# Kernel optimization log

Measured on AMD Instinct MI355X. Metric: run time of the kernel, lower is better.

The kernel has to match this reference:

```python
import jax, jax.numpy as jnp
import numpy as np

N = 50000
E = 640000
IN_DIM = 23
HID = 128
NUM_CLASS = 12


def setup_inputs() -> dict:
    key = jax.random.key(0)
    ks = jax.random.split(key, 12)
    x = jax.random.normal(ks[0], (N, IN_DIM), dtype=jnp.float32)
    edge_index = jax.random.randint(ks[1], (2, E), 0, N, dtype=jnp.int32)

    def glorot(k, shape):
        fan_in, fan_out = shape
        lim = np.sqrt(6.0 / (fan_in + fan_out)).astype(np.float32)
        return jax.random.uniform(k, shape, jnp.float32, -lim, lim)

    W1 = glorot(ks[2], (IN_DIM, HID)); b1 = jnp.zeros((HID,), jnp.float32)
    W2 = glorot(ks[3], (HID, HID));    b2 = jnp.zeros((HID,), jnp.float32)
    W3 = glorot(ks[4], (HID, HID));    b3 = jnp.zeros((HID,), jnp.float32)
    Wc1 = glorot(ks[5], (HID, 64));    bc1 = jnp.zeros((64,), jnp.float32)
    Wc2 = glorot(ks[6], (64, NUM_CLASS)); bc2 = jnp.zeros((NUM_CLASS,), jnp.float32)
    return {"x": x, "edge_index": edge_index,
            "W1": W1, "b1": b1, "W2": W2, "b2": b2, "W3": W3, "b3": b3,
            "Wc1": Wc1, "bc1": bc1, "Wc2": Wc2, "bc2": bc2}


def _gcn_norm(edge_index, n_nodes):
    # add self loops, compute symmetric normalization D^-1/2 (A+I) D^-1/2
    loop = jnp.arange(n_nodes, dtype=edge_index.dtype)
    src = jnp.concatenate([edge_index[0], loop])
    dst = jnp.concatenate([edge_index[1], loop])
    deg = jax.ops.segment_sum(jnp.ones_like(dst, dtype=jnp.float32), dst,
                              num_segments=n_nodes)
    dinv = jax.lax.rsqrt(deg)  # deg >= 1 due to self loops
    norm = dinv[src] * dinv[dst]  # [E + N]
    return src, dst, norm


def _gcn_layer(h, W, b, src, dst, norm, n_nodes):
    h = h @ W                          # linear (bias applied after aggregation, per PyG)
    msg = h[src] * norm[:, None]       # gather + scale
    out = jax.ops.segment_sum(msg, dst, num_segments=n_nodes)  # scatter-add
    return out + b


def reference(x, edge_index, W1, b1, W2, b2, W3, b3, Wc1, bc1, Wc2, bc2):
    n = x.shape[0]
    src, dst, norm = _gcn_norm(edge_index, n)
    h = jnp.tanh(_gcn_layer(x, W1, b1, src, dst, norm, n))
    h = jnp.tanh(_gcn_layer(h, W2, b2, src, dst, norm, n))
    h = jnp.tanh(_gcn_layer(h, W3, b3, src, dst, norm, n))
    # dropout is identity in eval mode
    out = h @ Wc1 + bc1
    out = out @ Wc2 + bc2
    return out
```

## Files before the change

### kernel.cpp

```cpp
#include <hip/hip_runtime.h>
#include <math.h>

#define NN 50000
#define EE 640000
#define IND 23
#define HID 128
#define MIDD 64
#define NCLS 12
#define NB 49
#define QS 32766.0f
#define INVQS (1.0f / 32766.0f)

typedef short short8v __attribute__((ext_vector_type(8)));
typedef float f32x4 __attribute__((ext_vector_type(4)));

__device__ __forceinline__ short f2bf(float f) {
    unsigned u = __float_as_uint(f);
    unsigned r = (u + 0x7FFFu + ((u >> 16) & 1u)) >> 16;
    return (short)r;
}
__device__ __forceinline__ float bf2f(short s) {
    return __uint_as_float(((unsigned)(unsigned short)s) << 16);
}


__global__ void k_count(const int* __restrict__ dst, int* __restrict__ cnt, int e) {
    int i = blockIdx.x * blockDim.x + threadIdx.x;
    if (i < e) atomicAdd(&cnt[dst[i]], 1);
}

__global__ __launch_bounds__(256) void k_scan_local(const int* __restrict__ cnt,
                                                    int* __restrict__ row_ptr,
                                                    float* __restrict__ dinv,
                                                    int* __restrict__ sums) {
    __shared__ int wtot[4];
    const int tid = threadIdx.x;
    const int wid = tid >> 6, lane = tid & 63;
    const int base = blockIdx.x * 1024 + tid * 4;
    int v[4];
#pragma unroll
    for (int t = 0; t < 4; ++t) {
        int i = base + t;
        v[t] = (i < NN) ? cnt[i] : 0;
        if (i < NN) dinv[i] = rsqrtf((float)v[t] + 1.0f);
    }
    int slocal = v[0] + v[1] + v[2] + v[3];
    int val = slocal;
#pragma unroll
    for (int off = 1; off < 64; off <<= 1) {
        int t = __shfl_up(val, off, 64);
        if (lane >= off) val += t;
    }
    if (lane == 63) wtot[wid] = val;
    __syncthreads();
    int woff = 0;
#pragma unroll
    for (int w = 0; w < 4; ++w) woff += (w < wid) ? wtot[w] : 0;
    int run = woff + val - slocal;
#pragma unroll
    for (int t = 0; t < 4; ++t) {
        int i = base + t;
        if (i < NN) row_ptr[i] = run;
        run += v[t];
    }
    if (tid == 255) sums[blockIdx.x] = woff + val;
}

__global__ void k_scan_sums(const int* __restrict__ sums, int* __restrict__ offs,
                            int* __restrict__ row_ptr) {
    const int lane = threadIdx.x;
    int v = (lane < NB) ? sums[lane] : 0;
    int val = v;
#pragma unroll
    for (int off = 1; off < 64; off <<= 1) {
        int t = __shfl_up(val, off, 64);
        if (lane >= off) val += t;
    }
    if (lane < NB) offs[lane] = val - v;
    if (lane == NB - 1) row_ptr[NN] = val;
}

__global__ __launch_bounds__(256) void k_scan_apply(int* __restrict__ row_ptr,
                                                    const int* __restrict__ offs,
                                                    int* __restrict__ cursor) {
    const int base = blockIdx.x * 1024 + threadIdx.x * 4;
    const int o = offs[blockIdx.x];
#pragma unroll
    for (int t = 0; t < 4; ++t) {
        int i = base + t;
        if (i < NN) {
            int rp = row_ptr[i] + o;
            row_ptr[i] = rp;
            cursor[i] = rp;
        }
    }
}

__global__ void k_fill(const int* __restrict__ src, const int* __restrict__ dst,
                       int* __restrict__ cursor, const float* __restrict__ dinv,
                       int2* __restrict__ e_sn, int e) {
    int i = blockIdx.x * blockDim.x + threadIdx.x;
    if (i < e) {
        int s = src[i];
        int d = dst[i];
        float w = dinv[s];
        int pos = atomicAdd(&cursor[d], 1);
        e_sn[pos] = make_int2(s, __float_as_int(w));
    }
}

__global__ __launch_bounds__(256) void k_pad(const float* __restrict__ x,
                                             const float* __restrict__ dinv,
                                             float* __restrict__ xp) {
    int i = blockIdx.x * 256 + threadIdx.x;
    int node = i >> 5, f = i & 31;
    xp[i] = (f < IND) ? x[node * IND + f] * dinv[node] : 0.f;
}

__global__ void k_wcc(const float* __restrict__ Wc1, const float* __restrict__ bc1,
                      const float* __restrict__ Wc2, const float* __restrict__ bc2,
                      float* __restrict__ Wcc, float* __restrict__ bcc) {
    int t = blockIdx.x * 256 + threadIdx.x;
    if (t < HID * NCLS) {
        int k = t / NCLS, c = t % NCLS;
        float s = 0.f;
#pragma unroll 8
        for (int j = 0; j < MIDD; ++j) s += Wc1[k * MIDD + j] * Wc2[j * NCLS + c];
        Wcc[t] = s;
    }
    if (t < NCLS) {
        float s = bc2[t];
#pragma unroll 8
        for (int j = 0; j < MIDD; ++j) s += bc1[j] * Wc2[j * NCLS + t];
        bcc[t] = s;
    }
}

__global__ void k_wsplit(const float* __restrict__ Wa, const float* __restrict__ Wb,
                         short* __restrict__ hiA, short* __restrict__ loA,
                         short* __restrict__ hiB, short* __restrict__ loB) {
    int i = blockIdx.x * 256 + threadIdx.x;
    const float* W = (blockIdx.y == 0) ? Wa : Wb;
    short* hi = (blockIdx.y == 0) ? hiA : hiB;
    short* lo = (blockIdx.y == 0) ? loA : loB;
    int k = i >> 7, c = i & 127;
    float w = W[i];
    short h = f2bf(w);
    short l = f2bf(w - bf2f(h));
    int t = k >> 5, g = (k >> 3) & 3, j = k & 7;
    int idx = ((t * 4 + g) * 128 + c) * 8 + j;
    hi[idx] = h;
    lo[idx] = l;
}

__global__ __launch_bounds__(256) void k_l1(const float* __restrict__ xp,
                                            const float* __restrict__ W1,
                                            const float* __restrict__ b1,
                                            const int* __restrict__ row_ptr,
                                            const int2* __restrict__ e_sn,
                                            const float* __restrict__ dinv,
                                            short* __restrict__ outq) {
    const int tid = threadIdx.x;
    const int i = blockIdx.x * 4 + (tid >> 6);
    const int lane = tid & 63;
    const int slot = lane >> 3;
    const int f = lane & 7;
    const float4* xp4 = (const float4*)xp;
    const int beg = row_ptr[i];
    const int deg = row_ptr[i + 1] - beg;
    float4 acc = make_float4(0.f, 0.f, 0.f, 0.f);
    for (int base = 0; base < deg; base += 64) {
        const int cnt = min(64, deg - base);
        int s_l = 0;
        if (lane < cnt) s_l = e_sn[beg + base + lane].x;
        int e = 0;
        for (; e + 8 <= cnt; e += 8) {
            int s = __shfl(s_l, e + slot, 64);
            float4 v = xp4[s * 8 + f];
            acc.x += v.x; acc.y += v.y; acc.z += v.z; acc.w += v.w;
        }
        if (e < cnt) {
            int s = __shfl(s_l, e + slot, 64);
            if (e + slot < cnt) {
                float4 v = xp4[s * 8 + f];
                acc.x += v.x; acc.y += v.y; acc.z += v.z; acc.w += v.w;
            }
        }
    }
#pragma unroll
    for (int off = 32; off >= 8; off >>= 1) {
        acc.x += __shfl_down(acc.x, off, 64);
        acc.y += __shfl_down(acc.y, off, 64);
        acc.z += __shfl_down(acc.z, off, 64);
        acc.w += __shfl_down(acc.w, off, 64);
    }
    const float di = dinv[i];
    if (lane < 8) {
        float4 v = xp4[i * 8 + lane];
        acc.x = (acc.x + v.x) * di; acc.y = (acc.y + v.y) * di;
        acc.z = (acc.z + v.z) * di; acc.w = (acc.w + v.w) * di;
    }
    float a0 = b1[lane], a1 = b1[lane + 64];
#pragma unroll
    for (int k = 0; k < IND; ++k) {
        float comp = ((k & 3) == 0) ? acc.x : ((k & 3) == 1) ? acc.y
                   : ((k & 3) == 2) ? acc.z : acc.w;
        float xk = __shfl(comp, k >> 2, 64);
        a0 += xk * W1[k * HID + lane];
        a1 += xk * W1[k * HID + lane + 64];
    }
    outq[i * HID + lane]      = (short)__float2int_rn(tanhf(a0) * QS);
    outq[i * HID + lane + 64] = (short)__float2int_rn(tanhf(a1) * QS);
}

__global__ __launch_bounds__(256) void k_aggq(const short* __restrict__ hq,
                                              const int* __restrict__ row_ptr,
                                              const int2* __restrict__ e_sn,
                                              const float* __restrict__ dinv,
                                              float* __restrict__ aggf) {
    const int tid = threadIdx.x;
    const int i = blockIdx.x * 4 + (tid >> 6);
    const int lane = tid & 63;
    const int slot = lane >> 4;
    const int f = lane & 15;
    const short8v* h8 = (const short8v*)hq;
    const int beg = row_ptr[i];
    const int deg = row_ptr[i + 1] - beg;
    float facc[8];
#pragma unroll
    for (int t = 0; t < 8; ++t) facc[t] = 0.f;
    for (int base = 0; base < deg; base += 64) {
        const int cnt = min(64, deg - base);
        int s_l = 0; float n_l = 0.f;
        if (lane < cnt) {
            int2 sn = e_sn[beg + base + lane];
            s_l = sn.x;
            n_l = __int_as_float(sn.y);
        }
        int e = 0;
#pragma unroll 4
        for (; e + 4 <= cnt; e += 4) {
            int s = __shfl(s_l, e + slot, 64);
            float nr = __shfl(n_l, e + slot, 64);
            short8v v = h8[s * 16 + f];
#pragma unroll
            for (int t = 0; t < 8; ++t) facc[t] += (float)v[t] * nr;
        }
        if (e < cnt) {
            int s = __shfl(s_l, e + slot, 64);
            float nr = __shfl(n_l, e + slot, 64);
            if (e + slot < cnt) {
                short8v v = h8[s * 16 + f];
#pragma unroll
                for (int t = 0; t < 8; ++t) facc[t] += (float)v[t] * nr;
            }
        }
    }
#pragma unroll
    for (int off = 32; off >= 16; off >>= 1)
#pragma unroll
        for (int t = 0; t < 8; ++t) facc[t] += __shfl_down(facc[t], off, 64);
    if (lane < 16) {
        const float di = dinv[i];
        const float sc = di * INVQS;
        short8v v = h8[i * 16 + lane];
        float4 o0, o1;
        o0.x = (facc[0] + di * (float)v[0]) * sc;
        o0.y = (facc[1] + di * (float)v[1]) * sc;
        o0.z = (facc[2] + di * (float)v[2]) * sc;
        o0.w = (facc[3] + di * (float)v[3]) * sc;
        o1.x = (facc[4] + di * (float)v[4]) * sc;
        o1.y = (facc[5] + di * (float)v[5]) * sc;
        o1.z = (facc[6] + di * (float)v[6]) * sc;
        o1.w = (facc[7] + di * (float)v[7]) * sc;
        ((float4*)aggf)[i * 32 + lane * 2]     = o0;
        ((float4*)aggf)[i * 32 + lane * 2 + 1] = o1;
    }
}

__device__ __forceinline__ void gemm_core(const float* __restrict__ hin,
                                          const short8v* __restrict__ whi8,
                                          const short8v* __restrict__ wlo8,
                                          int row, bool rv, int g, int c16,
                                          f32x4 acc[8]) {
#pragma unroll
    for (int t = 0; t < 4; ++t) {
        float4 a0 = make_float4(0.f, 0.f, 0.f, 0.f), a1 = a0;
        if (rv) {
            const float4* hp = (const float4*)&hin[row * HID + t * 32 + g * 8];
            a0 = hp[0]; a1 = hp[1];
        }
        float av[8];
        av[0] = a0.x; av[1] = a0.y; av[2] = a0.z; av[3] = a0.w;
        av[4] = a1.x; av[5] = a1.y; av[6] = a1.z; av[7] = a1.w;
        short8v ahi, alo;
#pragma unroll
        for (int j = 0; j < 8; ++j) {
            short h = f2bf(av[j]);
            ahi[j] = h;
            alo[j] = f2bf(av[j] - bf2f(h));
        }
        const int wb = (t * 4 + g) * 128 + c16;
#pragma unroll
        for (int n = 0; n < 8; ++n) {
            short8v bh = whi8[wb + n * 16];
            short8v bl = wlo8[wb + n * 16];
            acc[n] = __builtin_amdgcn_mfma_f32_16x16x32_bf16(ahi, bh, acc[n], 0, 0, 0);
            acc[n] = __builtin_amdgcn_mfma_f32_16x16x32_bf16(ahi, bl, acc[n], 0, 0, 0);
            acc[n] = __builtin_amdgcn_mfma_f32_16x16x32_bf16(alo, bh, acc[n], 0, 0, 0);
        }
    }
}

__global__ __launch_bounds__(256) void k_gemm_q(const float* __restrict__ hin,
                                                const short* __restrict__ whi,
                                                const short* __restrict__ wlo,
                                                const float* __restrict__ bias,
                                                short* __restrict__ qout) {
    const int tid = threadIdx.x;
    const int lane = tid & 63, w = tid >> 6;
    const int g = lane >> 4, c16 = lane & 15;
    const int rbase = blockIdx.x * 64 + w * 16;
    f32x4 acc[8];
#pragma unroll
    for (int n = 0; n < 8; ++n) acc[n] = f32x4{0.f, 0.f, 0.f, 0.f};
    gemm_core(hin, (const short8v*)whi, (const short8v*)wlo,
              rbase + c16, (rbase + c16) < NN, g, c16, acc);
#pragma unroll
    for (int n = 0; n < 8; ++n) {
        const float bb = bias[n * 16 + c16];
#pragma unroll
        for (int r = 0; r < 4; ++r) {
            int nd = rbase + 4 * g + r;
            if (nd < NN) {
                float v = tanhf(acc[n][r] + bb);
                qout[nd * HID + n * 16 + c16] = (short)__float2int_rn(v * QS);
            }
        }
    }
}

__global__ __launch_bounds__(256) void k_gemm_head(const float* __restrict__ hin,
                                                   const short* __restrict__ whi,
                                                   const short* __restrict__ wlo,
                                                   const float* __restrict__ bias,
                                                   const float* __restrict__ Wcc,
                                                   const float* __restrict__ bcc,
                                                   float* __restrict__ outp) {
    __shared__ float WccS[HID * NCLS + 16];
    const int tid = threadIdx.x;
    const int lane = tid & 63, w = tid >> 6;
    const int g = lane >> 4, c16 = lane & 15;
    const int rbase = blockIdx.x * 64 + w * 16;
    for (int t = tid; t < HID * NCLS; t += 256) WccS[t] = Wcc[t];
    if (tid < NCLS) WccS[HID * NCLS + tid] = bcc[tid];
    __syncthreads();
    f32x4 acc[8];
#pragma unroll
    for (int n = 0; n < 8; ++n) acc[n] = f32x4{0.f, 0.f, 0.f, 0.f};
    gemm_core(hin, (const short8v*)whi, (const short8v*)wlo,
              rbase + c16, (rbase + c16) < NN, g, c16, acc);
    float part[4][12];
#pragma unroll
    for (int r = 0; r < 4; ++r)
#pragma unroll
        for (int c = 0; c < 12; ++c) part[r][c] = 0.f;
#pragma unroll
    for (int n = 0; n < 8; ++n) {
        const float bb = bias[n * 16 + c16];
        const float4* wr = (const float4*)&WccS[(n * 16 + c16) * NCLS];
        float4 wa = wr[0], wb = wr[1], wc = wr[2];
#pragma unroll
        for (int r = 0; r < 4; ++r) {
            float v = tanhf(acc[n][r] + bb);
            part[r][0]  += v * wa.x; part[r][1]  += v * wa.y;
            part[r][2]  += v * wa.z; part[r][3]  += v * wa.w;
            part[r][4]  += v * wb.x; part[r][5]  += v * wb.y;
            part[r][6]  += v * wb.z; part[r][7]  += v * wb.w;
            part[r][8]  += v * wc.x; part[r][9]  += v * wc.y;
            part[r][10] += v * wc.z; part[r][11] += v * wc.w;
        }
    }
#pragma unroll
    for (int off = 8; off; off >>= 1)
#pragma unroll
        for (int r = 0; r < 4; ++r)
#pragma unroll
            for (int c = 0; c < 12; ++c)
                part[r][c] += __shfl_down(part[r][c], off, 64);
    if (c16 == 0) {
#pragma unroll
        for (int r = 0; r < 4; ++r) {
            int nd = rbase + 4 * g + r;
            if (nd < NN) {
                float4* op = (float4*)&outp[nd * NCLS];
                op[0] = make_float4(part[r][0] + WccS[HID * NCLS + 0],
                                    part[r][1] + WccS[HID * NCLS + 1],
                                    part[r][2] + WccS[HID * NCLS + 2],
                                    part[r][3] + WccS[HID * NCLS + 3]);
                op[1] = make_float4(part[r][4] + WccS[HID * NCLS + 4],
                                    part[r][5] + WccS[HID * NCLS + 5],
                                    part[r][6] + WccS[HID * NCLS + 6],
                                    part[r][7] + WccS[HID * NCLS + 7]);
                op[2] = make_float4(part[r][8] + WccS[HID * NCLS + 8],
                                    part[r][9] + WccS[HID * NCLS + 9],
                                    part[r][10] + WccS[HID * NCLS + 10],
                                    part[r][11] + WccS[HID * NCLS + 11]);
            }
        }
    }
}


extern "C" void kernel_launch(void* const* d_in, const int* in_sizes, int n_in,
                              void* d_out, int out_size, void* d_ws, size_t ws_size,
                              hipStream_t stream) {
    const float* x    = (const float*)d_in[0];
    const int*   edge = (const int*)d_in[1];
    const int*   src  = edge;
    const int*   dst  = edge + EE;
    const float* W1  = (const float*)d_in[2];  const float* b1  = (const float*)d_in[3];
    const float* W2  = (const float*)d_in[4];  const float* b2  = (const float*)d_in[5];
    const float* W3  = (const float*)d_in[6];  const float* b3  = (const float*)d_in[7];
    const float* Wc1 = (const float*)d_in[8];  const float* bc1 = (const float*)d_in[9];
    const float* Wc2 = (const float*)d_in[10]; const float* bc2 = (const float*)d_in[11];
    float* outp = (float*)d_out;

    char* p = (char*)d_ws;
    int*   cnt     = (int*)p;   p += 200064;
    int*   row_ptr = (int*)p;   p += 200064;
    float* dinv    = (float*)p; p += 200064;
    int*   sums    = (int*)p;   p += 256;
    int*   offs    = (int*)p;   p += 256;
    int2*  e_sn    = (int2*)p;  p += (size_t)EE * 8;
    float* xp      = (float*)p; p += (size_t)NN * 32 * 4;
    short* q       = (short*)p; p += (size_t)NN * HID * 2;
    float* aggf    = (float*)p; p += (size_t)NN * HID * 4;
    float* Wcc     = (float*)p; p += HID * NCLS * 4;
    float* bcc     = (float*)p; p += 256;
    short* w2hi    = (short*)p; p += 32768;
    short* w2lo    = (short*)p; p += 32768;
    short* w3hi    = (short*)p; p += 32768;
    short* w3lo    = (short*)p; p += 32768;

    hipMemsetAsync(cnt, 0, (size_t)NN * 4, stream);
    k_wcc       <<<(HID * NCLS + 255) / 256, 256, 0, stream>>>(Wc1, bc1, Wc2, bc2, Wcc, bcc);
    k_wsplit    <<<dim3(64, 2), 256, 0, stream>>>(W2, W3, w2hi, w2lo, w3hi, w3lo);
    k_count     <<<(EE + 255) / 256, 256, 0, stream>>>(dst, cnt, EE);
    k_scan_local<<<NB, 256, 0, stream>>>(cnt, row_ptr, dinv, sums);
    k_scan_sums <<<1, 64, 0, stream>>>(sums, offs, row_ptr);
    k_scan_apply<<<NB, 256, 0, stream>>>(row_ptr, offs, cnt);
    k_fill      <<<(EE + 255) / 256, 256, 0, stream>>>(src, dst, cnt, dinv, e_sn, EE);
    k_pad       <<<(NN * 32) / 256, 256, 0, stream>>>(x, dinv, xp);

    k_l1  <<<NN / 4, 256, 0, stream>>>(xp, W1, b1, row_ptr, e_sn, dinv, q);
    k_aggq     <<<NN / 4, 256, 0, stream>>>(q, row_ptr, e_sn, dinv, aggf);
    k_gemm_q   <<<(NN + 63) / 64, 256, 0, stream>>>(aggf, w2hi, w2lo, b2, q);
    k_aggq     <<<NN / 4, 256, 0, stream>>>(q, row_ptr, e_sn, dinv, aggf);
    k_gemm_head<<<(NN + 63) / 64, 256, 0, stream>>>(aggf, w3hi, w3lo, b3, Wcc, bcc, outp);
}
```

Baseline: 304.5 us.

## Fuse aggregation with MFMA GEMM per layer and merge preprocessing kernels

Each layer's gather-aggregation now writes a bf16 hi/lo split into LDS, and the same 512-thread block runs the MFMA GEMM and tanh over those 16 nodes. This removes the fp32 aggf round trip through global memory and two kernel launches. The preprocessing kernels are also merged (count+wcc+wsplit, fill+pad), and the scan-sums kernel is folded into the apply step, cutting launches further. In exchange, each GEMM block covers only 16 rows and reloads the weights per block, and the aggregation phase has fewer waves per node-group, which may lower latency hiding.

```diff
diff --git a/kernel.cpp b/kernel.cpp
--- a/kernel.cpp
+++ b/kernel.cpp
@@ -23,10 +23,56 @@
     return __uint_as_float(((unsigned)(unsigned short)s) << 16);
 }
 
-
-__global__ void k_count(const int* __restrict__ dst, int* __restrict__ cnt, int e) {
-    int i = blockIdx.x * blockDim.x + threadIdx.x;
-    if (i < e) atomicAdd(&cnt[dst[i]], 1);
+__global__ __launch_bounds__(256) void k_pre(const int* __restrict__ dst,
+                                             int* __restrict__ cnt,
+                                             const float* __restrict__ Wc1,
+                                             const float* __restrict__ bc1,
+                                             const float* __restrict__ Wc2,
+                                             const float* __restrict__ bc2,
+                                             float* __restrict__ Wcc,
+                                             float* __restrict__ bcc,
+                                             const float* __restrict__ W2,
+                                             const float* __restrict__ W3,
+                                             short* __restrict__ w2hi,
+                                             short* __restrict__ w2lo,
+                                             short* __restrict__ w3hi,
+                                             short* __restrict__ w3lo) {
+    const int bid = blockIdx.x;
+    const int tid = threadIdx.x;
+    if (bid < 2500) {
+        int i = bid * 256 + tid;
+        if (i < EE) atomicAdd(&cnt[dst[i]], 1);
+        return;
+    }
+    if (bid < 2506) {
+        int t = (bid - 2500) * 256 + tid;
+        if (t < HID * NCLS) {
+            int k = t / NCLS, c = t % NCLS;
+            float s = 0.f;
+#pragma unroll 8
+            for (int j = 0; j < MIDD; ++j) s += Wc1[k * MIDD + j] * Wc2[j * NCLS + c];
+            Wcc[t] = s;
+        }
+        if (t < NCLS) {
+            float s = bc2[t];
+#pragma unroll 8
+            for (int j = 0; j < MIDD; ++j) s += bc1[j] * Wc2[j * NCLS + t];
+            bcc[t] = s;
+        }
+        return;
+    }
+    int bb = bid - 2506;
+    const float* W = (bb < 64) ? W2 : W3;
+    short* hi = (bb < 64) ? w2hi : w3hi;
+    short* lo = (bb < 64) ? w2lo : w3lo;
+    int i = (bb & 63) * 256 + tid;
+    int k = i >> 7, c = i & 127;
+    float w = W[i];
+    short h = f2bf(w);
+    short l = f2bf(w - bf2f(h));
+    int t = k >> 5, g = (k >> 3) & 3, j = k & 7;
+    hi[((t * 4 + g) * 128 + c) * 8 + j] = h;
+    lo[((t * 4 + g) * 128 + c) * 8 + j] = l;
 }
 
 __global__ __launch_bounds__(256) void k_scan_local(const int* __restrict__ cnt,
@@ -66,25 +112,27 @@
     if (tid == 255) sums[blockIdx.x] = woff + val;
 }
 
-__global__ void k_scan_sums(const int* __restrict__ sums, int* __restrict__ offs,
-                            int* __restrict__ row_ptr) {
-    const int lane = threadIdx.x;
-    int v = (lane < NB) ? sums[lane] : 0;
-    int val = v;
-#pragma unroll
-    for (int off = 1; off < 64; off <<= 1) {
-        int t = __shfl_up(val, off, 64);
-        if (lane >= off) val += t;
-    }
-    if (lane < NB) offs[lane] = val - v;
-    if (lane == NB - 1) row_ptr[NN] = val;
-}
-
-__global__ __launch_bounds__(256) void k_scan_apply(int* __restrict__ row_ptr,
-                                                    const int* __restrict__ offs,
-                                                    int* __restrict__ cursor) {
-    const int base = blockIdx.x * 1024 + threadIdx.x * 4;
-    const int o = offs[blockIdx.x];
+__global__ __launch_bounds__(256) void k_scan_apply2(int* __restrict__ row_ptr,
+                                                     const int* __restrict__ sums,
+                                                     int* __restrict__ cursor) {
+    __shared__ int so;
+    const int tid = threadIdx.x;
+    if (tid < 64) {
+        int a = (tid < (int)blockIdx.x) ? sums[tid] : 0;
+        int b = (tid < NB) ? sums[tid] : 0;
+#pragma unroll
+        for (int off = 32; off; off >>= 1) {
+            a += __shfl_down(a, off, 64);
+            b += __shfl_down(b, off, 64);
+        }
+        if (tid == 0) {
+            so = a;
+            if (blockIdx.x == NB - 1) row_ptr[NN] = b;
+        }
+    }
+    __syncthreads();
+    const int o = so;
+    const int base = blockIdx.x * 1024 + tid * 4;
 #pragma unroll
     for (int t = 0; t < 4; ++t) {
         int i = base + t;
@@ -96,61 +144,29 @@
     }
 }
 
-__global__ void k_fill(const int* __restrict__ src, const int* __restrict__ dst,
-                       int* __restrict__ cursor, const float* __restrict__ dinv,
-                       int2* __restrict__ e_sn, int e) {
-    int i = blockIdx.x * blockDim.x + threadIdx.x;
-    if (i < e) {
-        int s = src[i];
-        int d = dst[i];
-        float w = dinv[s];
-        int pos = atomicAdd(&cursor[d], 1);
-        e_sn[pos] = make_int2(s, __float_as_int(w));
-    }
-}
-
-__global__ __launch_bounds__(256) void k_pad(const float* __restrict__ x,
-                                             const float* __restrict__ dinv,
-                                             float* __restrict__ xp) {
-    int i = blockIdx.x * 256 + threadIdx.x;
+__global__ __launch_bounds__(256) void k_fillpad(const int* __restrict__ src,
+                                                 const int* __restrict__ dst,
+                                                 int* __restrict__ cursor,
+                                                 const float* __restrict__ dinv,
+                                                 int2* __restrict__ e_sn,
+                                                 const float* __restrict__ x,
+                                                 float* __restrict__ xp) {
+    const int bid = blockIdx.x;
+    const int tid = threadIdx.x;
+    if (bid < 2500) {
+        int i = bid * 256 + tid;
+        if (i < EE) {
+            int s = src[i];
+            int d = dst[i];
+            float w = dinv[s];
+            int pos = atomicAdd(&cursor[d], 1);
+            e_sn[pos] = make_int2(s, __float_as_int(w));
+        }
+        return;
+    }
+    int i = (bid - 2500) * 256 + tid;
     int node = i >> 5, f = i & 31;
     xp[i] = (f < IND) ? x[node * IND + f] * dinv[node] : 0.f;
-}
-
-__global__ void k_wcc(const float* __restrict__ Wc1, const float* __restrict__ bc1,
-                      const float* __restrict__ Wc2, const float* __restrict__ bc2,
-                      float* __restrict__ Wcc, float* __restrict__ bcc) {
-    int t = blockIdx.x * 256 + threadIdx.x;
-    if (t < HID * NCLS) {
-        int k = t / NCLS, c = t % NCLS;
-        float s = 0.f;
-#pragma unroll 8
-        for (int j = 0; j < MIDD; ++j) s += Wc1[k * MIDD + j] * Wc2[j * NCLS + c];
-        Wcc[t] = s;
-    }
-    if (t < NCLS) {
-        float s = bc2[t];
-#pragma unroll 8
-        for (int j = 0; j < MIDD; ++j) s += bc1[j] * Wc2[j * NCLS + t];
-        bcc[t] = s;
-    }
-}
-
-__global__ void k_wsplit(const float* __restrict__ Wa, const float* __restrict__ Wb,
-                         short* __restrict__ hiA, short* __restrict__ loA,
-                         short* __restrict__ hiB, short* __restrict__ loB) {
-    int i = blockIdx.x * 256 + threadIdx.x;
-    const float* W = (blockIdx.y == 0) ? Wa : Wb;
-    short* hi = (blockIdx.y == 0) ? hiA : hiB;
-    short* lo = (blockIdx.y == 0) ? loA : loB;
-    int k = i >> 7, c = i & 127;
-    float w = W[i];
-    short h = f2bf(w);
-    short l = f2bf(w - bf2f(h));
-    int t = k >> 5, g = (k >> 3) & 3, j = k & 7;
-    int idx = ((t * 4 + g) * 128 + c) * 8 + j;
-    hi[idx] = h;
-    lo[idx] = l;
 }
 
 __global__ __launch_bounds__(256) void k_l1(const float* __restrict__ xp,
@@ -213,201 +229,193 @@
     outq[i * HID + lane + 64] = (short)__float2int_rn(tanhf(a1) * QS);
 }
 
-__global__ __launch_bounds__(256) void k_aggq(const short* __restrict__ hq,
-                                              const int* __restrict__ row_ptr,
-                                              const int2* __restrict__ e_sn,
-                                              const float* __restrict__ dinv,
-                                              float* __restrict__ aggf) {
-    const int tid = threadIdx.x;
-    const int i = blockIdx.x * 4 + (tid >> 6);
-    const int lane = tid & 63;
+__device__ __forceinline__ void agg_to_lds(const short8v* __restrict__ h8,
+                                           const int* __restrict__ row_ptr,
+                                           const int2* __restrict__ e_sn,
+                                           const float* __restrict__ dinv,
+                                           int nb, int wv, int lane,
+                                           short8v* hiS, short8v* loS) {
     const int slot = lane >> 4;
-    const int f = lane & 15;
-    const short8v* h8 = (const short8v*)hq;
-    const int beg = row_ptr[i];
-    const int deg = row_ptr[i + 1] - beg;
-    float facc[8];
-#pragma unroll
-    for (int t = 0; t < 8; ++t) facc[t] = 0.f;
-    for (int base = 0; base < deg; base += 64) {
-        const int cnt = min(64, deg - base);
-        int s_l = 0; float n_l = 0.f;
-        if (lane < cnt) {
-            int2 sn = e_sn[beg + base + lane];
-            s_l = sn.x;
-            n_l = __int_as_float(sn.y);
-        }
-        int e = 0;
+    for (int jn = 0; jn < 2; ++jn) {
+        const int r = wv * 2 + jn;
+        const int i = nb + r;
+        const int beg = row_ptr[i];
+        const int deg = row_ptr[i + 1] - beg;
+        float facc[8];
+#pragma unroll
+        for (int t = 0; t < 8; ++t) facc[t] = 0.f;
+        for (int base = 0; base < deg; base += 64) {
+            const int cnt = min(64, deg - base);
+            int s_l = 0; float n_l = 0.f;
+            if (lane < cnt) {
+                int2 sn = e_sn[beg + base + lane];
+                s_l = sn.x;
+                n_l = __int_as_float(sn.y);
+            }
+            int e = 0;
 #pragma unroll 4
-        for (; e + 4 <= cnt; e += 4) {
-            int s = __shfl(s_l, e + slot, 64);
-            float nr = __shfl(n_l, e + slot, 64);
-            short8v v = h8[s * 16 + f];
-#pragma unroll
-            for (int t = 0; t < 8; ++t) facc[t] += (float)v[t] * nr;
-        }
-        if (e < cnt) {
-            int s = __shfl(s_l, e + slot, 64);
-            float nr = __shfl(n_l, e + slot, 64);
-            if (e + slot < cnt) {
-                short8v v = h8[s * 16 + f];
+            for (; e + 4 <= cnt; e += 4) {
+                int s = __shfl(s_l, e + slot, 64);
+                float nr = __shfl(n_l, e + slot, 64);
+                short8v v = h8[s * 16 + (lane & 15)];
 #pragma unroll
                 for (int t = 0; t < 8; ++t) facc[t] += (float)v[t] * nr;
             }
-        }
-    }
-#pragma unroll
-    for (int off = 32; off >= 16; off >>= 1)
-#pragma unroll
-        for (int t = 0; t < 8; ++t) facc[t] += __shfl_down(facc[t], off, 64);
-    if (lane < 16) {
-        const float di = dinv[i];
-        const float sc = di * INVQS;
-        short8v v = h8[i * 16 + lane];
-        float4 o0, o1;
-        o0.x = (facc[0] + di * (float)v[0]) * sc;
-        o0.y = (facc[1] + di * (float)v[1]) * sc;
-        o0.z = (facc[2] + di * (float)v[2]) * sc;
-        o0.w = (facc[3] + di * (float)v[3]) * sc;
-        o1.x = (facc[4] + di * (float)v[4]) * sc;
-        o1.y = (facc[5] + di * (float)v[5]) * sc;
-        o1.z = (facc[6] + di * (float)v[6]) * sc;
-        o1.w = (facc[7] + di * (float)v[7]) * sc;
-        ((float4*)aggf)[i * 32 + lane * 2]     = o0;
-        ((float4*)aggf)[i * 32 + lane * 2 + 1] = o1;
-    }
-}
-
-__device__ __forceinline__ void gemm_core(const float* __restrict__ hin,
-                                          const short8v* __restrict__ whi8,
-                                          const short8v* __restrict__ wlo8,
-                                          int row, bool rv, int g, int c16,
-                                          f32x4 acc[8]) {
+            if (e < cnt) {
+                int s = __shfl(s_l, e + slot, 64);
+                float nr = __shfl(n_l, e + slot, 64);
+                if (e + slot < cnt) {
+                    short8v v = h8[s * 16 + (lane & 15)];
+#pragma unroll
+                    for (int t = 0; t < 8; ++t) facc[t] += (float)v[t] * nr;
+                }
+            }
+        }
+#pragma unroll
+        for (int off = 32; off >= 16; off >>= 1)
+#pragma unroll
+            for (int t = 0; t < 8; ++t) facc[t] += __shfl_down(facc[t], off, 64);
+        if (lane < 16) {
+            const float di = dinv[i];
+            const float sc = di * INVQS;
+            short8v v = h8[i * 16 + lane];
+            short8v hi8, lo8;
+#pragma unroll
+            for (int t = 0; t < 8; ++t) {
+                float o = (facc[t] + di * (float)v[t]) * sc;
+                short h = f2bf(o);
+                hi8[t] = h;
+                lo8[t] = f2bf(o - bf2f(h));
+            }
+            hiS[r * 17 + lane] = hi8;
+            loS[r * 17 + lane] = lo8;
+        }
+    }
+}
+
+__global__ __launch_bounds__(512) void k_layer_q(const short* __restrict__ hq,
+                                                 const int* __restrict__ row_ptr,
+                                                 const int2* __restrict__ e_sn,
+                                                 const float* __restrict__ dinv,
+                                                 const short* __restrict__ whi,
+                                                 const short* __restrict__ wlo,
+                                                 const float* __restrict__ bias,
+                                                 short* __restrict__ qout) {
+    __shared__ short8v hiS[16 * 17];
+    __shared__ short8v loS[16 * 17];
+    __shared__ short8v q2v[16 * 17];
+    const int tid = threadIdx.x;
+    const int wv = tid >> 6, lane = tid & 63;
+    const int nb = blockIdx.x * 16;
+    const short8v* h8 = (const short8v*)hq;
+    agg_to_lds(h8, row_ptr, e_sn, dinv, nb, wv, lane, hiS, loS);
+    __syncthreads();
+    const int g = lane >> 4, c16 = lane & 15;
+    const short8v* whi8 = (const short8v*)whi;
+    const short8v* wlo8 = (const short8v*)wlo;
+    f32x4 acc = f32x4{0.f, 0.f, 0.f, 0.f};
 #pragma unroll
     for (int t = 0; t < 4; ++t) {
-        float4 a0 = make_float4(0.f, 0.f, 0.f, 0.f), a1 = a0;
-        if (rv) {
-            const float4* hp = (const float4*)&hin[row * HID + t * 32 + g * 8];
-            a0 = hp[0]; a1 = hp[1];
-        }
-        float av[8];
-        av[0] = a0.x; av[1] = a0.y; av[2] = a0.z; av[3] = a0.w;
-        av[4] = a1.x; av[5] = a1.y; av[6] = a1.z; av[7] = a1.w;
-        short8v ahi, alo;
-#pragma unroll
-        for (int j = 0; j < 8; ++j) {
-            short h = f2bf(av[j]);
-            ahi[j] = h;
-            alo[j] = f2bf(av[j] - bf2f(h));
-        }
-        const int wb = (t * 4 + g) * 128 + c16;
-#pragma unroll
-        for (int n = 0; n < 8; ++n) {
-            short8v bh = whi8[wb + n * 16];
-            short8v bl = wlo8[wb + n * 16];
-            acc[n] = __builtin_amdgcn_mfma_f32_16x16x32_bf16(ahi, bh, acc[n], 0, 0, 0);
-            acc[n] = __builtin_amdgcn_mfma_f32_16x16x32_bf16(ahi, bl, acc[n], 0, 0, 0);
-            acc[n] = __builtin_amdgcn_mfma_f32_16x16x32_bf16(alo, bh, acc[n], 0, 0, 0);
-        }
-    }
-}
-
-__global__ __launch_bounds__(256) void k_gemm_q(const float* __restrict__ hin,
-                                                const short* __restrict__ whi,
-                                                const short* __restrict__ wlo,
-                                                const float* __restrict__ bias,
-                                                short* __restrict__ qout) {
-    const int tid = threadIdx.x;
-    const int lane = tid & 63, w = tid >> 6;
+        short8v ah = hiS[c16 * 17 + t * 4 + g];
+        short8v al = loS[c16 * 17 + t * 4 + g];
+        const int wb = (t * 4 + g) * 128 + wv * 16 + c16;
+        short8v bh = whi8[wb];
+        short8v bl = wlo8[wb];
+        acc = __builtin_amdgcn_mfma_f32_16x16x32_bf16(ah, bh, acc, 0, 0, 0);
+        acc = __builtin_amdgcn_mfma_f32_16x16x32_bf16(ah, bl, acc, 0, 0, 0);
+        acc = __builtin_amdgcn_mfma_f32_16x16x32_bf16(al, bh, acc, 0, 0, 0);
+    }
+    const float bb = bias[wv * 16 + c16];
+    short* q2s = (short*)q2v;
+#pragma unroll
+    for (int r2 = 0; r2 < 4; ++r2) {
+        float v = tanhf(acc[r2] + bb);
+        q2s[(4 * g + r2) * 136 + wv * 16 + c16] = (short)__float2int_rn(v * QS);
+    }
+    __syncthreads();
+    if (tid < 256) {
+        int row = tid >> 4, seg = tid & 15;
+        ((short8v*)qout)[(nb + row) * 16 + seg] = q2v[row * 17 + seg];
+    }
+}
+
+__global__ __launch_bounds__(512) void k_layer_head(const short* __restrict__ hq,
+                                                    const int* __restrict__ row_ptr,
+                                                    const int2* __restrict__ e_sn,
+                                                    const float* __restrict__ dinv,
+                                                    const short* __restrict__ whi,
+                                                    const short* __restrict__ wlo,
+                                                    const float* __restrict__ bias,
+                                                    const float* __restrict__ Wcc,
+                                                    const float* __restrict__ bcc,
+                                                    float* __restrict__ outp) {
+    __shared__ short8v hiS[16 * 17];
+    __shared__ short8v loS[16 * 17];
+    __shared__ float WccS[HID * NCLS];
+    __shared__ float bccS[NCLS];
+    __shared__ float psum[8][16][NCLS];
+    const int tid = threadIdx.x;
+    const int wv = tid >> 6, lane = tid & 63;
+    const int nb = blockIdx.x * 16;
+    const short8v* h8 = (const short8v*)hq;
+    for (int t = tid; t < HID * NCLS; t += 512) WccS[t] = Wcc[t];
+    if (tid < NCLS) bccS[tid] = bcc[tid];
+    agg_to_lds(h8, row_ptr, e_sn, dinv, nb, wv, lane, hiS, loS);
+    __syncthreads();
     const int g = lane >> 4, c16 = lane & 15;
-    const int rbase = blockIdx.x * 64 + w * 16;
-    f32x4 acc[8];
-#pragma unroll
-    for (int n = 0; n < 8; ++n) acc[n] = f32x4{0.f, 0.f, 0.f, 0.f};
-    gemm_core(hin, (const short8v*)whi, (const short8v*)wlo,
-              rbase + c16, (rbase + c16) < NN, g, c16, acc);
-#pragma unroll
-    for (int n = 0; n < 8; ++n) {
-        const float bb = bias[n * 16 + c16];
-#pragma unroll
-        for (int r = 0; r < 4; ++r) {
-            int nd = rbase + 4 * g + r;
-            if (nd < NN) {
-                float v = tanhf(acc[n][r] + bb);
-                qout[nd * HID + n * 16 + c16] = (short)__float2int_rn(v * QS);
-            }
-        }
-    }
-}
-
-__global__ __launch_bounds__(256) void k_gemm_head(const float* __restrict__ hin,
-                                                   const short* __restrict__ whi,
-                                                   const short* __restrict__ wlo,
-                                                   const float* __restrict__ bias,
-                                                   const float* __restrict__ Wcc,
-                                                   const float* __restrict__ bcc,
-                                                   float* __restrict__ outp) {
-    __shared__ float WccS[HID * NCLS + 16];
-    const int tid = threadIdx.x;
-    const int lane = tid & 63, w = tid >> 6;
-    const int g = lane >> 4, c16 = lane & 15;
-    const int rbase = blockIdx.x * 64 + w * 16;
-    for (int t = tid; t < HID * NCLS; t += 256) WccS[t] = Wcc[t];
-    if (tid < NCLS) WccS[HID * NCLS + tid] = bcc[tid];
-    __syncthreads();
-    f32x4 acc[8];
-#pragma unroll
-    for (int n = 0; n < 8; ++n) acc[n] = f32x4{0.f, 0.f, 0.f, 0.f};
-    gemm_core(hin, (const short8v*)whi, (const short8v*)wlo,
-              rbase + c16, (rbase + c16) < NN, g, c16, acc);
-    float part[4][12];
-#pragma unroll
-    for (int r = 0; r < 4; ++r)
-#pragma unroll
-        for (int c = 0; c < 12; ++c) part[r][c] = 0.f;
-#pragma unroll
-    for (int n = 0; n < 8; ++n) {
-        const float bb = bias[n * 16 + c16];
-        const float4* wr = (const float4*)&WccS[(n * 16 + c16) * NCLS];
-        float4 wa = wr[0], wb = wr[1], wc = wr[2];
-#pragma unroll
-        for (int r = 0; r < 4; ++r) {
-            float v = tanhf(acc[n][r] + bb);
-            part[r][0]  += v * wa.x; part[r][1]  += v * wa.y;
-            part[r][2]  += v * wa.z; part[r][3]  += v * wa.w;
-            part[r][4]  += v * wb.x; part[r][5]  += v * wb.y;
-            part[r][6]  += v * wb.z; part[r][7]  += v * wb.w;
-            part[r][8]  += v * wc.x; part[r][9]  += v * wc.y;
-            part[r][10] += v * wc.z; part[r][11] += v * wc.w;
-        }
+    const short8v* whi8 = (const short8v*)whi;
+    const short8v* wlo8 = (const short8v*)wlo;
+    f32x4 acc = f32x4{0.f, 0.f, 0.f, 0.f};
+#pragma unroll
+    for (int t = 0; t < 4; ++t) {
+        short8v ah = hiS[c16 * 17 + t * 4 + g];
+        short8v al = loS[c16 * 17 + t * 4 + g];
+        const int wb = (t * 4 + g) * 128 + wv * 16 + c16;
+        short8v bh = whi8[wb];
+        short8v bl = wlo8[wb];
+        acc = __builtin_amdgcn_mfma_f32_16x16x32_bf16(ah, bh, acc, 0, 0, 0);
+        acc = __builtin_amdgcn_mfma_f32_16x16x32_bf16(ah, bl, acc, 0, 0, 0);
+        acc = __builtin_amdgcn_mfma_f32_16x16x32_bf16(al, bh, acc, 0, 0, 0);
+    }
+    const float bb = bias[wv * 16 + c16];
+    float part[4][NCLS];
+#pragma unroll
+    for (int r2 = 0; r2 < 4; ++r2)
+#pragma unroll
+        for (int c = 0; c < NCLS; ++c) part[r2][c] = 0.f;
+    const float4* wr = (const float4*)&WccS[(wv * 16 + c16) * NCLS];
+    float4 wa = wr[0], wb2 = wr[1], wc = wr[2];
+#pragma unroll
+    for (int r2 = 0; r2 < 4; ++r2) {
+        float v = tanhf(acc[r2] + bb);
+        part[r2][0]  += v * wa.x;  part[r2][1]  += v * wa.y;
+        part[r2][2]  += v * wa.z;  part[r2][3]  += v * wa.w;
+        part[r2][4]  += v * wb2.x; part[r2][5]  += v * wb2.y;
+        part[r2][6]  += v * wb2.z; part[r2][7]  += v * wb2.w;
+        part[r2][8]  += v * wc.x;  part[r2][9]  += v * wc.y;
+        part[r2][10] += v * wc.z;  part[r2][11] += v * wc.w;
     }
 #pragma unroll
     for (int off = 8; off; off >>= 1)
 #pragma unroll
-        for (int r = 0; r < 4; ++r)
-#pragma unroll
-            for (int c = 0; c < 12; ++c)
-                part[r][c] += __shfl_down(part[r][c], off, 64);
+        for (int r2 = 0; r2 < 4; ++r2)
+#pragma unroll
+            for (int c = 0; c < NCLS; ++c)
+                part[r2][c] += __shfl_down(part[r2][c], off, 64);
     if (c16 == 0) {
 #pragma unroll
-        for (int r = 0; r < 4; ++r) {
-            int nd = rbase + 4 * g + r;
-            if (nd < NN) {
-                float4* op = (float4*)&outp[nd * NCLS];
-                op[0] = make_float4(part[r][0] + WccS[HID * NCLS + 0],
-                                    part[r][1] + WccS[HID * NCLS + 1],
-                                    part[r][2] + WccS[HID * NCLS + 2],
-                                    part[r][3] + WccS[HID * NCLS + 3]);
-                op[1] = make_float4(part[r][4] + WccS[HID * NCLS + 4],
-                                    part[r][5] + WccS[HID * NCLS + 5],
-                                    part[r][6] + WccS[HID * NCLS + 6],
-                                    part[r][7] + WccS[HID * NCLS + 7]);
-                op[2] = make_float4(part[r][8] + WccS[HID * NCLS + 8],
-                                    part[r][9] + WccS[HID * NCLS + 9],
-                                    part[r][10] + WccS[HID * NCLS + 10],
-                                    part[r][11] + WccS[HID * NCLS + 11]);
-            }
-        }
+        for (int r2 = 0; r2 < 4; ++r2)
+#pragma unroll
+            for (int c = 0; c < NCLS; ++c)
+                psum[wv][4 * g + r2][c] = part[r2][c];
+    }
+    __syncthreads();
+    if (tid < 16 * NCLS) {
+        int row = tid / NCLS, c = tid % NCLS;
+        float s = bccS[c];
+#pragma unroll
+        for (int w = 0; w < 8; ++w) s += psum[w][row][c];
+        outp[(nb + row) * NCLS + c] = s;
     }
 }
 
@@ -431,11 +439,10 @@
     int*   row_ptr = (int*)p;   p += 200064;
     float* dinv    = (float*)p; p += 200064;
     int*   sums    = (int*)p;   p += 256;
-    int*   offs    = (int*)p;   p += 256;
     int2*  e_sn    = (int2*)p;  p += (size_t)EE * 8;
     float* xp      = (float*)p; p += (size_t)NN * 32 * 4;
-    short* q       = (short*)p; p += (size_t)NN * HID * 2;
-    float* aggf    = (float*)p; p += (size_t)NN * HID * 4;
+    short* q1      = (short*)p; p += (size_t)NN * HID * 2;
+    short* q2      = (short*)p; p += (size_t)NN * HID * 2;
     float* Wcc     = (float*)p; p += HID * NCLS * 4;
     float* bcc     = (float*)p; p += 256;
     short* w2hi    = (short*)p; p += 32768;
@@ -444,18 +451,14 @@
     short* w3lo    = (short*)p; p += 32768;
 
     hipMemsetAsync(cnt, 0, (size_t)NN * 4, stream);
-    k_wcc       <<<(HID * NCLS + 255) / 256, 256, 0, stream>>>(Wc1, bc1, Wc2, bc2, Wcc, bcc);
-    k_wsplit    <<<dim3(64, 2), 256, 0, stream>>>(W2, W3, w2hi, w2lo, w3hi, w3lo);
-    k_count     <<<(EE + 255) / 256, 256, 0, stream>>>(dst, cnt, EE);
-    k_scan_local<<<NB, 256, 0, stream>>>(cnt, row_ptr, dinv, sums);
-    k_scan_sums <<<1, 64, 0, stream>>>(sums, offs, row_ptr);
-    k_scan_apply<<<NB, 256, 0, stream>>>(row_ptr, offs, cnt);
-    k_fill      <<<(EE + 255) / 256, 256, 0, stream>>>(src, dst, cnt, dinv, e_sn, EE);
-    k_pad       <<<(NN * 32) / 256, 256, 0, stream>>>(x, dinv, xp);
-
-    k_l1  <<<NN / 4, 256, 0, stream>>>(xp, W1, b1, row_ptr, e_sn, dinv, q);
-    k_aggq     <<<NN / 4, 256, 0, stream>>>(q, row_ptr, e_sn, dinv, aggf);
-    k_gemm_q   <<<(NN + 63) / 64, 256, 0, stream>>>(aggf, w2hi, w2lo, b2, q);
-    k_aggq     <<<NN / 4, 256, 0, stream>>>(q, row_ptr, e_sn, dinv, aggf);
-    k_gemm_head<<<(NN + 63) / 64, 256, 0, stream>>>(aggf, w3hi, w3lo, b3, Wcc, bcc, outp);
-}
+    k_pre        <<<2634, 256, 0, stream>>>(dst, cnt, Wc1, bc1, Wc2, bc2, Wcc, bcc,
+                                            W2, W3, w2hi, w2lo, w3hi, w3lo);
+    k_scan_local <<<NB, 256, 0, stream>>>(cnt, row_ptr, dinv, sums);
+    k_scan_apply2<<<NB, 256, 0, stream>>>(row_ptr, sums, cnt);
+    k_fillpad    <<<8750, 256, 0, stream>>>(src, dst, cnt, dinv, e_sn, x, xp);
+
+    k_l1        <<<NN / 4, 256, 0, stream>>>(xp, W1, b1, row_ptr, e_sn, dinv, q1);
+    k_layer_q   <<<NN / 16, 512, 0, stream>>>(q1, row_ptr, e_sn, dinv, w2hi, w2lo, b2, q2);
+    k_layer_head<<<NN / 16, 512, 0, stream>>>(q2, row_ptr, e_sn, dinv, w3hi, w3lo, b3,
+                                              Wcc, bcc, outp);
+}
```

New measurement: 329.2 us. +8.1%, slower.
